# Optimization experiments

Measured on AMD Instinct MI355X. Metric: run time of the kernel, lower is better.

The kernel has to match this reference:

```python
import jax, jax.numpy as jnp
import numpy as np

VOCAB, BLOCK, D, H, L = 50257, 2048, 768, 12, 4
B, T = 1, 2048
DH = D // H


def setup_inputs() -> dict:
    key = jax.random.key(0)
    ks = jax.random.split(key, 16)
    s = 0.02
    return {
        "tokens": jax.random.randint(ks[0], (B, T), 0, VOCAB),
        "wte": jax.random.normal(ks[1], (VOCAB, D), jnp.float32) * s,
        "wpe": jax.random.normal(ks[2], (BLOCK, D), jnp.float32) * s,
        "ln1_w": jnp.ones((L, D), jnp.float32),
        "ln1_b": jnp.zeros((L, D), jnp.float32),
        "qkv_w": jax.random.normal(ks[3], (L, D, 3 * D), jnp.float32) * s,
        "qkv_b": jnp.zeros((L, 3 * D), jnp.float32),
        "proj_w": jax.random.normal(ks[4], (L, D, D), jnp.float32) * s,
        "proj_b": jnp.zeros((L, D), jnp.float32),
        "ln2_w": jnp.ones((L, D), jnp.float32),
        "ln2_b": jnp.zeros((L, D), jnp.float32),
        "fc_w": jax.random.normal(ks[5], (L, D, 4 * D), jnp.float32) * s,
        "fc_b": jnp.zeros((L, 4 * D), jnp.float32),
        "fcp_w": jax.random.normal(ks[6], (L, 4 * D, D), jnp.float32) * s,
        "fcp_b": jnp.zeros((L, D), jnp.float32),
        "lnf_w": jnp.ones((D,), jnp.float32),
        "lnf_b": jnp.zeros((D,), jnp.float32),
    }


def _ln(x, w, b, eps=1e-5):
    m = jnp.mean(x, axis=-1, keepdims=True)
    v = jnp.mean((x - m) ** 2, axis=-1, keepdims=True)
    return (x - m) * jax.lax.rsqrt(v + eps) * w + b


def _attn(x, wq, bq, wp, bp):
    Bq, Tq, _ = x.shape
    qkv = x @ wq + bq  # [B,T,3D]
    q, k, v = jnp.split(qkv, 3, axis=-1)
    q = q.reshape(Bq, Tq, H, DH).transpose(0, 2, 1, 3)  # [B,H,T,dh]
    k = k.reshape(Bq, Tq, H, DH).transpose(0, 2, 1, 3)
    v = v.reshape(Bq, Tq, H, DH).transpose(0, 2, 1, 3)
    w = jnp.einsum("bhqd,bhkd->bhqk", q, k) / np.sqrt(DH).astype(np.float32)
    mask = jnp.tril(jnp.ones((Tq, Tq), bool))
    w = jnp.where(mask, w, -jnp.inf)
    w = jax.nn.softmax(w, axis=-1)
    y = jnp.einsum("bhqk,bhkd->bhqd", w, v)
    y = y.transpose(0, 2, 1, 3).reshape(Bq, Tq, D)
    return y @ wp + bp


def reference(tokens, wte, wpe, ln1_w, ln1_b, qkv_w, qkv_b, proj_w, proj_b,
              ln2_w, ln2_b, fc_w, fc_b, fcp_w, fcp_b, lnf_w, lnf_b):
    x = wte[tokens] + wpe[jnp.arange(tokens.shape[1])]  # [B,T,D]
    for l in range(L):
        x = x + _attn(_ln(x, ln1_w[l], ln1_b[l]), qkv_w[l], qkv_b[l], proj_w[l], proj_b[l])
        h = _ln(x, ln2_w[l], ln2_b[l]) @ fc_w[l] + fc_b[l]
        h = jax.nn.gelu(h, approximate=True)
        x = x + h @ fcp_w[l] + fcp_b[l]
    x = _ln(x, lnf_w, lnf_b)
    logits = x @ wte.T  # tied lm_head, [B,T,V]
    return logits
```

## Files before the change

### kernel.cpp

```cpp
#include <hip/hip_runtime.h>
#include <hip/hip_bf16.h>

#define TSEQ   2048
#define DMODEL 768
#define NHEAD  12
#define DHEAD  64
#define NLAYER 4
#define VOCAB  50257
#define VPAD   50304

typedef __attribute__((ext_vector_type(8))) short short8;
typedef __attribute__((ext_vector_type(4))) float f32x4;
typedef unsigned short ushort_t;

union F8 { short8 v; unsigned long long q[2]; };

__device__ __forceinline__ float b2f(ushort_t u) {
  return __uint_as_float(((unsigned)u) << 16);
}
__device__ __forceinline__ ushort_t f2bu(float f) {
  unsigned u = __float_as_uint(f);
  unsigned r = (u + 0x7fffu + ((u >> 16) & 1u)) >> 16;
  return (ushort_t)r;
}

__device__ __forceinline__ void gload_lds16(const void* g, void* l) {
  __builtin_amdgcn_global_load_lds(
      (const __attribute__((address_space(1))) unsigned int*)g,
      (__attribute__((address_space(3))) unsigned int*)l, 16, 0, 0);
}

__global__ __launch_bounds__(256) void embed_kernel(
    const int* __restrict__ tok, const float* __restrict__ wte,
    const float* __restrict__ wpe, float* __restrict__ x) {
  int i = blockIdx.x * 256 + threadIdx.x;
  int t = i / DMODEL;
  int d = i - t * DMODEL;
  x[i] = wte[tok[t] * DMODEL + d] + wpe[i];
}

__global__ __launch_bounds__(256) void cvt_kernel(
    const float* __restrict__ in, ushort_t* __restrict__ out, int n4) {
  for (int i = blockIdx.x * 256 + threadIdx.x; i < n4; i += gridDim.x * 256) {
    float4 f = reinterpret_cast<const float4*>(in)[i];
    ushort4 o;
    o.x = f2bu(f.x); o.y = f2bu(f.y); o.z = f2bu(f.z); o.w = f2bu(f.w);
    reinterpret_cast<ushort4*>(out)[i] = o;
  }
}

__global__ __launch_bounds__(256) void tcvt_kernel(
    const float* __restrict__ W, ushort_t* __restrict__ Wt, int K, int N,
    long long wstride) {
  W  += (size_t)blockIdx.z * wstride;
  Wt += (size_t)blockIdx.z * wstride;
  __shared__ float Ts[32][33];
  int n0 = blockIdx.x * 32, k0 = blockIdx.y * 32;
  int tx = threadIdx.x & 31, ty = threadIdx.x >> 5;
#pragma unroll
  for (int s = 0; s < 4; ++s)
    Ts[ty + 8 * s][tx] = W[(size_t)(k0 + ty + 8 * s) * N + n0 + tx];
  __syncthreads();
#pragma unroll
  for (int s = 0; s < 4; ++s)
    Wt[(size_t)(n0 + ty + 8 * s) * K + k0 + tx] = f2bu(Ts[tx][ty + 8 * s]);
}

__global__ __launch_bounds__(256) void ln_kernel(
    const float* __restrict__ x, const float* __restrict__ w,
    const float* __restrict__ b, ushort_t* __restrict__ out) {
  int row = blockIdx.x;
  int t = threadIdx.x;
  const float* xr = x + row * DMODEL;
  float v0 = xr[t], v1 = xr[t + 256], v2 = xr[t + 512];
  float s = v0 + v1 + v2;
  float q = v0 * v0 + v1 * v1 + v2 * v2;
#pragma unroll
  for (int off = 32; off >= 1; off >>= 1) {
    s += __shfl_xor(s, off);
    q += __shfl_xor(q, off);
  }
  __shared__ float rs[4], rq[4];
  int wid = t >> 6;
  if ((t & 63) == 0) { rs[wid] = s; rq[wid] = q; }
  __syncthreads();
  s = rs[0] + rs[1] + rs[2] + rs[3];
  q = rq[0] + rq[1] + rq[2] + rq[3];
  float mean = s * (1.f / DMODEL);
  float var  = q * (1.f / DMODEL) - mean * mean;
  float rstd = rsqrtf(var + 1e-5f);
  ushort_t* o = out + row * DMODEL;
  o[t]       = f2bu((v0 - mean) * rstd * w[t]       + b[t]);
  o[t + 256] = f2bu((v1 - mean) * rstd * w[t + 256] + b[t + 256]);
  o[t + 512] = f2bu((v2 - mean) * rstd * w[t + 512] + b[t + 512]);
}

template <int TM, int TN, bool BIAS, bool RES, bool GELU, bool OUTBF16, bool XSWZ>
__global__ __launch_bounds__(256) void mm_kernel(
    const ushort_t* __restrict__ A, const ushort_t* __restrict__ Bt,
    const float* __restrict__ bias, const float* __restrict__ res,
    void* __restrict__ outp, int N, int K, int nrowblk, int nwg) {
  constexpr int HM = TM / 2, HN = TN / 2, FI = TM / 32, FJ = TN / 32;
  constexpr int NCA = TM / 32, NCB = TN / 32;
  __shared__ ushort_t Asm[TM * 64];
  __shared__ ushort_t Bsm[TN * 64];
  const int tid = threadIdx.x;
  const int lane = tid & 63, wid = tid >> 6;
  const int wr = wid >> 1, wc = wid & 1;
  const int l15 = lane & 15, c4 = lane >> 4;
  const int qb0 = (c4 >> 1) << 4;
  const int qb1 = qb0 + 32;
  const int e8 = (c4 & 1) * 8;

  int bid = blockIdx.x;
  if (XSWZ) { int q = nwg >> 3; bid = (bid & 7) * q + (bid >> 3); }
  const int rowb = bid % nrowblk, colb = bid / nrowblk;
  const int rowA0 = rowb * TM, colB0 = colb * TN;

  int ap0[FI], ax[FI], bp0[FJ], bx[FJ];
#pragma unroll
  for (int i = 0; i < FI; ++i) {
    int r = wr * HM + i * 16 + l15;
    ap0[i] = r * 128 + e8; ax[i] = (r & 7) << 4;
  }
#pragma unroll
  for (int j = 0; j < FJ; ++j) {
    int r = wc * HN + j * 16 + l15;
    bp0[j] = r * 128 + e8; bx[j] = (r & 7) << 4;
  }

  const ushort_t* asrc[NCA]; ushort_t* adst[NCA];
  const ushort_t* bsrc[NCB]; ushort_t* bdst[NCB];
#pragma unroll
  for (int s = 0; s < NCA; ++s) {
    int ci = tid + s * 256;
    int row = ci >> 3;
    int logch = (ci & 7) ^ (row & 7);
    asrc[s] = A + (size_t)(rowA0 + row) * K + logch * 8;
    adst[s] = Asm + ci * 8;
  }
#pragma unroll
  for (int s = 0; s < NCB; ++s) {
    int ci = tid + s * 256;
    int row = ci >> 3;
    int logch = (ci & 7) ^ (row & 7);
    bsrc[s] = Bt + (size_t)(colB0 + row) * K + logch * 8;
    bdst[s] = Bsm + ci * 8;
  }

  f32x4 acc[FI][FJ] = {};
  const char* Ab = (const char*)Asm;
  const char* Bb = (const char*)Bsm;

  for (int kt = 0; kt < K; kt += 64) {
    __syncthreads();
#pragma unroll
    for (int s = 0; s < NCA; ++s) gload_lds16(asrc[s] + kt, adst[s]);
#pragma unroll
    for (int s = 0; s < NCB; ++s) gload_lds16(bsrc[s] + kt, bdst[s]);
    __syncthreads();
#pragma unroll
    for (int kk = 0; kk < 2; ++kk) {
      const int k64 = kk * 64;
      short8 a[FI], b[FJ];
#pragma unroll
      for (int i = 0; i < FI; ++i) {
        F8 f;
        f.q[0] = *(const unsigned long long*)(Ab + ap0[i] + ((k64 + qb0) ^ ax[i]));
        f.q[1] = *(const unsigned long long*)(Ab + ap0[i] + ((k64 + qb1) ^ ax[i]));
        a[i] = f.v;
      }
#pragma unroll
      for (int j = 0; j < FJ; ++j) {
        F8 f;
        f.q[0] = *(const unsigned long long*)(Bb + bp0[j] + ((k64 + qb0) ^ bx[j]));
        f.q[1] = *(const unsigned long long*)(Bb + bp0[j] + ((k64 + qb1) ^ bx[j]));
        b[j] = f.v;
      }
#pragma unroll
      for (int i = 0; i < FI; ++i)
#pragma unroll
        for (int j = 0; j < FJ; ++j)
          acc[i][j] = __builtin_amdgcn_mfma_f32_16x16x32_bf16(a[i], b[j], acc[i][j], 0, 0, 0);
    }
  }

#pragma unroll
  for (int i = 0; i < FI; ++i) {
    const int rbase = rowA0 + wr * HM + i * 16 + c4 * 4;
#pragma unroll
    for (int j = 0; j < FJ; ++j) {
      const int col = colB0 + wc * HN + j * 16 + l15;
      if (col < N) {
        float bv = BIAS ? bias[col] : 0.f;
#pragma unroll
        for (int t = 0; t < 4; ++t) {
          float v = acc[i][j][t] + bv;
          if (GELU) {
            float z = 1.5957691216057308f * (v + 0.044715f * v * v * v);
            float th = 1.f - 2.f / (__expf(z) + 1.f);
            v = 0.5f * v * (1.f + th);
          }
          size_t o = (size_t)(rbase + t) * N + col;
          if (RES)          ((float*)outp)[o] = v + res[o];
          else if (OUTBF16) ((ushort_t*)outp)[o] = f2bu(v);
          else              ((float*)outp)[o] = v;
        }
      }
    }
  }
}

__global__ __launch_bounds__(256) void fattn_kernel(
    const ushort_t* __restrict__ qkv, ushort_t* __restrict__ y) {
  const int id = blockIdx.x;
  const int w32 = id / NHEAD;
  const int h = id - w32 * NHEAD;
  const int qb = (w32 & 1) ? (w32 >> 1) : (31 - (w32 >> 1));
  const int q0 = qb * 64;

  __shared__ ushort_t Ksm[64 * 64];
  __shared__ ushort_t Vsm[64 * 64];
  __shared__ ushort_t Psm[4 * 16 * 64];

  const int tid = threadIdx.x;
  const int lane = tid & 63, wv = tid >> 6;
  const int l15 = lane & 15, c4 = lane >> 4;
  const int r7 = l15 & 7;

  const ushort_t* qrow = qkv + (size_t)(q0 + wv * 16 + l15) * (3 * DMODEL) + h * DHEAD;
  const short8 qf0 = *(const short8*)(qrow + c4 * 8);
  const short8 qf1 = *(const short8*)(qrow + 32 + c4 * 8);

  const ushort_t* ksrc[2]; ushort_t* kdst[2];
#pragma unroll
  for (int s = 0; s < 2; ++s) {
    int row = wv * 16 + s * 8 + (lane >> 3);
    int cs = (lane & 7) ^ (row & 7);
    ksrc[s] = qkv + (size_t)row * (3 * DMODEL) + DMODEL + h * DHEAD + cs * 8;
    kdst[s] = Ksm + ((wv * 2 + s) * 64) * 8;
  }
  const int vk = tid & 63, vd0 = (tid >> 6) * 8;
  const ushort_t* vsrc = qkv + (size_t)vk * (3 * DMODEL) + 2 * DMODEL + h * DHEAD;
  const int vkoff = ((vk >> 3) << 3) + (vk & 7);

  float m[4] = {-1e30f, -1e30f, -1e30f, -1e30f};
  float l[4] = {};
  f32x4 acc[4] = {};
  ushort_t* Pw = Psm + wv * 1024;

  for (int k0 = 0; k0 <= q0; k0 += 64) {
    const size_t koff = (size_t)k0 * (3 * DMODEL);
    short8 v0 = *(const short8*)(vsrc + koff + vd0);
    short8 v1 = *(const short8*)(vsrc + koff + vd0 + 32);
    __syncthreads();
#pragma unroll
    for (int s = 0; s < 2; ++s) gload_lds16(ksrc[s] + koff, kdst[s]);
#pragma unroll
    for (int j = 0; j < 8; ++j) {
      int d = vd0 + j;
      Vsm[d * 64 + (vkoff ^ ((d & 7) << 3))] = (ushort_t)v0[j];
      int d2 = d + 32;
      Vsm[d2 * 64 + (vkoff ^ ((d2 & 7) << 3))] = (ushort_t)v1[j];
    }
    __syncthreads();

    f32x4 sv[4];
#pragma unroll
    for (int kt = 0; kt < 4; ++kt) {
      const ushort_t* krow = Ksm + (kt * 16 + l15) * 64;
      short8 kb0 = *(const short8*)(krow + ((c4 ^ r7) << 3));
      short8 kb1 = *(const short8*)(krow + (((4 + c4) ^ r7) << 3));
      f32x4 s = {};
      s = __builtin_amdgcn_mfma_f32_16x16x32_bf16(qf0, kb0, s, 0, 0, 0);
      s = __builtin_amdgcn_mfma_f32_16x16x32_bf16(qf1, kb1, s, 0, 0, 0);
      sv[kt] = s * 0.125f;
    }
    if (k0 == q0) {
#pragma unroll
      for (int kt = 0; kt < 4; ++kt)
#pragma unroll
        for (int r = 0; r < 4; ++r)
          if (kt * 16 + l15 > wv * 16 + c4 * 4 + r) sv[kt][r] = -1e30f;
    }

#pragma unroll
    for (int r = 0; r < 4; ++r) {
      float mv = fmaxf(fmaxf(sv[0][r], sv[1][r]), fmaxf(sv[2][r], sv[3][r]));
      mv = fmaxf(mv, __shfl_xor(mv, 1));
      mv = fmaxf(mv, __shfl_xor(mv, 2));
      mv = fmaxf(mv, __shfl_xor(mv, 4));
      mv = fmaxf(mv, __shfl_xor(mv, 8));
      float nm = fmaxf(m[r], mv);
      float sc = __expf(m[r] - nm);
      m[r] = nm;
      const int row = c4 * 4 + r;
      float sum = 0.f;
#pragma unroll
      for (int kt = 0; kt < 4; ++kt) {
        float p = __expf(sv[kt][r] - nm);
        sum += p;
        Pw[row * 64 + (((kt * 2 + (l15 >> 3)) ^ (row & 7)) << 3) + (l15 & 7)] = f2bu(p);
      }
      sum += __shfl_xor(sum, 1);
      sum += __shfl_xor(sum, 2);
      sum += __shfl_xor(sum, 4);
      sum += __shfl_xor(sum, 8);
      l[r] = l[r] * sc + sum;
#pragma unroll
      for (int j = 0; j < 4; ++j) acc[j][r] *= sc;
    }

    const ushort_t* prow = Pw + l15 * 64;
    short8 pa0 = *(const short8*)(prow + ((c4 ^ r7) << 3));
    short8 pa1 = *(const short8*)(prow + (((4 + c4) ^ r7) << 3));
#pragma unroll
    for (int j = 0; j < 4; ++j) {
      const ushort_t* vrow = Vsm + (j * 16 + l15) * 64;
      short8 vb0 = *(const short8*)(vrow + ((c4 ^ r7) << 3));
      short8 vb1 = *(const short8*)(vrow + (((4 + c4) ^ r7) << 3));
      acc[j] = __builtin_amdgcn_mfma_f32_16x16x32_bf16(pa0, vb0, acc[j], 0, 0, 0);
      acc[j] = __builtin_amdgcn_mfma_f32_16x16x32_bf16(pa1, vb1, acc[j], 0, 0, 0);
    }
  }

  float inv[4];
#pragma unroll
  for (int r = 0; r < 4; ++r) inv[r] = 1.f / l[r];
#pragma unroll
  for (int j = 0; j < 4; ++j)
#pragma unroll
    for (int r = 0; r < 4; ++r)
      y[(size_t)(q0 + wv * 16 + c4 * 4 + r) * DMODEL + h * DHEAD + j * 16 + l15] =
          f2bu(acc[j][r] * inv[r]);
}

extern "C" void kernel_launch(void* const* d_in, const int* in_sizes, int n_in,
                              void* d_out, int out_size, void* d_ws, size_t ws_size,
                              hipStream_t stream) {
  const int*   tokens = (const int*)d_in[0];
  const float* wte    = (const float*)d_in[1];
  const float* wpe    = (const float*)d_in[2];
  const float* ln1_w  = (const float*)d_in[3];
  const float* ln1_b  = (const float*)d_in[4];
  const float* qkv_w  = (const float*)d_in[5];
  const float* qkv_b  = (const float*)d_in[6];
  const float* proj_w = (const float*)d_in[7];
  const float* proj_b = (const float*)d_in[8];
  const float* ln2_w  = (const float*)d_in[9];
  const float* ln2_b  = (const float*)d_in[10];
  const float* fc_w   = (const float*)d_in[11];
  const float* fc_b   = (const float*)d_in[12];
  const float* fcp_w  = (const float*)d_in[13];
  const float* fcp_b  = (const float*)d_in[14];
  const float* lnf_w  = (const float*)d_in[15];
  const float* lnf_b  = (const float*)d_in[16];
  float* out = (float*)d_out;

  char* p = (char*)d_ws;
  auto alloc = [&](size_t bytes) { char* r = p; p += (bytes + 255) & ~(size_t)255; return r; };
  float*    x     = (float*)alloc((size_t)TSEQ * DMODEL * 4);
  ushort_t* lnb   = (ushort_t*)alloc((size_t)TSEQ * DMODEL * 2);
  ushort_t* buf   = (ushort_t*)alloc((size_t)TSEQ * 4 * DMODEL * 2);
  ushort_t* wteb  = (ushort_t*)alloc((size_t)VPAD * DMODEL * 2);
  ushort_t* qkvwt = (ushort_t*)alloc((size_t)NLAYER * 3 * DMODEL * DMODEL * 2);
  ushort_t* projwt= (ushort_t*)alloc((size_t)NLAYER * DMODEL * DMODEL * 2);
  ushort_t* fcwt  = (ushort_t*)alloc((size_t)NLAYER * 4 * DMODEL * DMODEL * 2);
  ushort_t* fcpwt = (ushort_t*)alloc((size_t)NLAYER * 4 * DMODEL * DMODEL * 2);
  ushort_t* qkvb  = buf;
  ushort_t* yb    = buf + (size_t)TSEQ * 3 * DMODEL;
  ushort_t* hfcb  = buf;

  dim3 b256(256);

  cvt_kernel<<<dim3(4096), b256, 0, stream>>>(wte, wteb, VOCAB * DMODEL / 4);
  tcvt_kernel<<<dim3(3 * DMODEL / 32, DMODEL / 32, NLAYER), b256, 0, stream>>>(
      qkv_w, qkvwt, DMODEL, 3 * DMODEL, (long long)3 * DMODEL * DMODEL);
  tcvt_kernel<<<dim3(DMODEL / 32, DMODEL / 32, NLAYER), b256, 0, stream>>>(
      proj_w, projwt, DMODEL, DMODEL, (long long)DMODEL * DMODEL);
  tcvt_kernel<<<dim3(4 * DMODEL / 32, DMODEL / 32, NLAYER), b256, 0, stream>>>(
      fc_w, fcwt, DMODEL, 4 * DMODEL, (long long)4 * DMODEL * DMODEL);
  tcvt_kernel<<<dim3(DMODEL / 32, 4 * DMODEL / 32, NLAYER), b256, 0, stream>>>(
      fcp_w, fcpwt, 4 * DMODEL, DMODEL, (long long)4 * DMODEL * DMODEL);

  embed_kernel<<<dim3(TSEQ * DMODEL / 256), b256, 0, stream>>>(tokens, wte, wpe, x);

  for (int l = 0; l < NLAYER; ++l) {
    ln_kernel<<<dim3(TSEQ), b256, 0, stream>>>(x, ln1_w + l * DMODEL, ln1_b + l * DMODEL, lnb);
    mm_kernel<128, 128, true, false, false, true, false><<<dim3(18 * 16), b256, 0, stream>>>(
        lnb, qkvwt + (size_t)l * 3 * DMODEL * DMODEL, qkv_b + (size_t)l * 3 * DMODEL,
        nullptr, qkvb, 3 * DMODEL, DMODEL, 16, 288);
    fattn_kernel<<<dim3(32 * NHEAD), b256, 0, stream>>>(qkvb, yb);
    mm_kernel<64, 64, true, true, false, false, false><<<dim3(12 * 32), b256, 0, stream>>>(
        yb, projwt + (size_t)l * DMODEL * DMODEL, proj_b + (size_t)l * DMODEL,
        x, x, DMODEL, DMODEL, 32, 384);
    ln_kernel<<<dim3(TSEQ), b256, 0, stream>>>(x, ln2_w + l * DMODEL, ln2_b + l * DMODEL, lnb);
    mm_kernel<128, 128, true, false, true, true, false><<<dim3(24 * 16), b256, 0, stream>>>(
        lnb, fcwt + (size_t)l * 4 * DMODEL * DMODEL, fc_b + (size_t)l * 4 * DMODEL,
        nullptr, hfcb, 4 * DMODEL, DMODEL, 16, 384);
    mm_kernel<64, 64, true, true, false, false, false><<<dim3(12 * 32), b256, 0, stream>>>(
        hfcb, fcpwt + (size_t)l * DMODEL * 4 * DMODEL, fcp_b + (size_t)l * DMODEL,
        x, x, DMODEL, 4 * DMODEL, 32, 384);
  }

  ln_kernel<<<dim3(TSEQ), b256, 0, stream>>>(x, lnf_w, lnf_b, lnb);
  mm_kernel<128, 128, false, false, false, false, true><<<dim3(393 * 16), b256, 0, stream>>>(
      lnb, wteb, nullptr, nullptr, out, VOCAB, DMODEL, 16, 393 * 16);
}
```

Before: 1.085 ms.

## Double-buffer LDS tiles in GEMM kernel with configurable K-tile depth

The GEMM kernel now keeps two LDS buffers for its A and B tiles. It prefetches the next K-tile into the idle buffer while running MFMA on the current one, so each K step needs one barrier instead of two. A BK template parameter is added, with a generalized XOR swizzle for 4 or 8 chunks per row. The 128x128 GEMMs, including the large LM head, use BK=32 so total LDS stays the same, and the 64x64 ones keep BK=64. The cost is twice as many loop iterations and barriers on the 128x128 kernels, and the prefetch depends on the barrier's implicit wait on outstanding loads.

New measurement: 1.106 ms. No clear change (+1.9%).

```diff
diff --git a/kernel.cpp b/kernel.cpp
--- a/kernel.cpp
+++ b/kernel.cpp
@@ -95,21 +95,23 @@
   o[t + 512] = f2bu((v2 - mean) * rstd * w[t + 512] + b[t + 512]);
 }
 
-template <int TM, int TN, bool BIAS, bool RES, bool GELU, bool OUTBF16, bool XSWZ>
+template <int TM, int TN, int BK, bool BIAS, bool RES, bool GELU, bool OUTBF16, bool XSWZ>
 __global__ __launch_bounds__(256) void mm_kernel(
     const ushort_t* __restrict__ A, const ushort_t* __restrict__ Bt,
     const float* __restrict__ bias, const float* __restrict__ res,
     void* __restrict__ outp, int N, int K, int nrowblk, int nwg) {
   constexpr int HM = TM / 2, HN = TN / 2, FI = TM / 32, FJ = TN / 32;
-  constexpr int NCA = TM / 32, NCB = TN / 32;
-  __shared__ ushort_t Asm[TM * 64];
-  __shared__ ushort_t Bsm[TN * 64];
+  constexpr int CH = BK / 8;
+  constexpr int LOGCH = (CH == 4) ? 2 : 3;
+  constexpr int NCA = TM * CH / 256, NCB = TN * CH / 256;
+  constexpr int ABUF = TM * BK, BBUF = TN * BK;
+  __shared__ ushort_t Asm[2][ABUF];
+  __shared__ ushort_t Bsm[2][BBUF];
   const int tid = threadIdx.x;
   const int lane = tid & 63, wid = tid >> 6;
   const int wr = wid >> 1, wc = wid & 1;
   const int l15 = lane & 15, c4 = lane >> 4;
-  const int qb0 = (c4 >> 1) << 4;
-  const int qb1 = qb0 + 32;
+  const int qc = c4 >> 1;
   const int e8 = (c4 & 1) * 8;
 
   int bid = blockIdx.x;
@@ -117,64 +119,74 @@
   const int rowb = bid % nrowblk, colb = bid / nrowblk;
   const int rowA0 = rowb * TM, colB0 = colb * TN;
 
-  int ap0[FI], ax[FI], bp0[FJ], bx[FJ];
+  auto swz = [](int row) { return ((row * CH) >> 3) & (CH - 1); };
+
+  int ap0[FI], axr[FI], bp0[FJ], bxr[FJ];
 #pragma unroll
   for (int i = 0; i < FI; ++i) {
     int r = wr * HM + i * 16 + l15;
-    ap0[i] = r * 128 + e8; ax[i] = (r & 7) << 4;
+    ap0[i] = r * (CH * 16) + e8; axr[i] = swz(r);
   }
 #pragma unroll
   for (int j = 0; j < FJ; ++j) {
     int r = wc * HN + j * 16 + l15;
-    bp0[j] = r * 128 + e8; bx[j] = (r & 7) << 4;
-  }
-
-  const ushort_t* asrc[NCA]; ushort_t* adst[NCA];
-  const ushort_t* bsrc[NCB]; ushort_t* bdst[NCB];
+    bp0[j] = r * (CH * 16) + e8; bxr[j] = swz(r);
+  }
+
+  const ushort_t* asrc[NCA]; int adst[NCA];
+  const ushort_t* bsrc[NCB]; int bdst[NCB];
 #pragma unroll
   for (int s = 0; s < NCA; ++s) {
     int ci = tid + s * 256;
-    int row = ci >> 3;
-    int logch = (ci & 7) ^ (row & 7);
+    int row = ci >> LOGCH;
+    int logch = (ci & (CH - 1)) ^ swz(row);
     asrc[s] = A + (size_t)(rowA0 + row) * K + logch * 8;
-    adst[s] = Asm + ci * 8;
+    adst[s] = ci * 8;
   }
 #pragma unroll
   for (int s = 0; s < NCB; ++s) {
     int ci = tid + s * 256;
-    int row = ci >> 3;
-    int logch = (ci & 7) ^ (row & 7);
+    int row = ci >> LOGCH;
+    int logch = (ci & (CH - 1)) ^ swz(row);
     bsrc[s] = Bt + (size_t)(colB0 + row) * K + logch * 8;
-    bdst[s] = Bsm + ci * 8;
+    bdst[s] = ci * 8;
   }
 
   f32x4 acc[FI][FJ] = {};
-  const char* Ab = (const char*)Asm;
-  const char* Bb = (const char*)Bsm;
-
-  for (int kt = 0; kt < K; kt += 64) {
+  const int nt = K / BK;
+
+#pragma unroll
+  for (int s = 0; s < NCA; ++s) gload_lds16(asrc[s], &Asm[0][adst[s]]);
+#pragma unroll
+  for (int s = 0; s < NCB; ++s) gload_lds16(bsrc[s], &Bsm[0][bdst[s]]);
+
+  for (int t = 0; t < nt; ++t) {
+    const int cur = t & 1;
     __syncthreads();
-#pragma unroll
-    for (int s = 0; s < NCA; ++s) gload_lds16(asrc[s] + kt, adst[s]);
-#pragma unroll
-    for (int s = 0; s < NCB; ++s) gload_lds16(bsrc[s] + kt, bdst[s]);
-    __syncthreads();
-#pragma unroll
-    for (int kk = 0; kk < 2; ++kk) {
-      const int k64 = kk * 64;
+    if (t + 1 < nt) {
+      const int kt = (t + 1) * BK;
+#pragma unroll
+      for (int s = 0; s < NCA; ++s) gload_lds16(asrc[s] + kt, &Asm[cur ^ 1][adst[s]]);
+#pragma unroll
+      for (int s = 0; s < NCB; ++s) gload_lds16(bsrc[s] + kt, &Bsm[cur ^ 1][bdst[s]]);
+    }
+    const char* Ab = (const char*)&Asm[cur][0];
+    const char* Bb = (const char*)&Bsm[cur][0];
+#pragma unroll
+    for (int kk = 0; kk < BK / 32; ++kk) {
       short8 a[FI], b[FJ];
 #pragma unroll
       for (int i = 0; i < FI; ++i) {
         F8 f;
-        f.q[0] = *(const unsigned long long*)(Ab + ap0[i] + ((k64 + qb0) ^ ax[i]));
-        f.q[1] = *(const unsigned long long*)(Ab + ap0[i] + ((k64 + qb1) ^ ax[i]));
+        f.q[0] = *(const unsigned long long*)(Ab + ap0[i] + (((kk * 4 + qc) ^ axr[i]) << 4));
+        f.q[1] = *(const unsigned long long*)(Ab + ap0[i] + (((kk * 4 + qc + 2) ^ axr[i]) << 4));
         a[i] = f.v;
       }
 #pragma unroll
       for (int j = 0; j < FJ; ++j) {
         F8 f;
-        f.q[0] = *(const unsigned long long*)(Bb + bp0[j] + ((k64 + qb0) ^ bx[j]));
-        f.q[1] = *(const unsigned long long*)(Bb + bp0[j] + ((k64 + qb1) ^ bx[j]));
+        f.q[0] = *(const unsigned long long*)(Bb + bp0[j] + (((kk * 4 + qc) ^ bxr[j]) << 4));
+        f.q[1] = *(const unsigned long long*)(Bb + bp0[j] + (((kk * 4 + qc + 2) ^ bxr[j]) << 4));
         b[j] = f.v;
       }
 #pragma unroll
@@ -387,23 +399,23 @@
 
   for (int l = 0; l < NLAYER; ++l) {
     ln_kernel<<<dim3(TSEQ), b256, 0, stream>>>(x, ln1_w + l * DMODEL, ln1_b + l * DMODEL, lnb);
-    mm_kernel<128, 128, true, false, false, true, false><<<dim3(18 * 16), b256, 0, stream>>>(
+    mm_kernel<128, 128, 32, true, false, false, true, false><<<dim3(18 * 16), b256, 0, stream>>>(
         lnb, qkvwt + (size_t)l * 3 * DMODEL * DMODEL, qkv_b + (size_t)l * 3 * DMODEL,
         nullptr, qkvb, 3 * DMODEL, DMODEL, 16, 288);
     fattn_kernel<<<dim3(32 * NHEAD), b256, 0, stream>>>(qkvb, yb);
-    mm_kernel<64, 64, true, true, false, false, false><<<dim3(12 * 32), b256, 0, stream>>>(
+    mm_kernel<64, 64, 64, true, true, false, false, false><<<dim3(12 * 32), b256, 0, stream>>>(
         yb, projwt + (size_t)l * DMODEL * DMODEL, proj_b + (size_t)l * DMODEL,
         x, x, DMODEL, DMODEL, 32, 384);
     ln_kernel<<<dim3(TSEQ), b256, 0, stream>>>(x, ln2_w + l * DMODEL, ln2_b + l * DMODEL, lnb);
-    mm_kernel<128, 128, true, false, true, true, false><<<dim3(24 * 16), b256, 0, stream>>>(
+    mm_kernel<128, 128, 32, true, false, true, true, false><<<dim3(24 * 16), b256, 0, stream>>>(
         lnb, fcwt + (size_t)l * 4 * DMODEL * DMODEL, fc_b + (size_t)l * 4 * DMODEL,
         nullptr, hfcb, 4 * DMODEL, DMODEL, 16, 384);
-    mm_kernel<64, 64, true, true, false, false, false><<<dim3(12 * 32), b256, 0, stream>>>(
+    mm_kernel<64, 64, 64, true, true, false, false, false><<<dim3(12 * 32), b256, 0, stream>>>(
         hfcb, fcpwt + (size_t)l * DMODEL * 4 * DMODEL, fcp_b + (size_t)l * DMODEL,
         x, x, DMODEL, 4 * DMODEL, 32, 384);
   }
 
   ln_kernel<<<dim3(TSEQ), b256, 0, stream>>>(x, lnf_w, lnf_b, lnb);
-  mm_kernel<128, 128, false, false, false, false, true><<<dim3(393 * 16), b256, 0, stream>>>(
+  mm_kernel<128, 128, 32, false, false, false, false, true><<<dim3(393 * 16), b256, 0, stream>>>(
       lnb, wteb, nullptr, nullptr, out, VOCAB, DMODEL, 16, 393 * 16);
 }
```

## Use dedicated 256x256 tiled kernel for LM head logits GEMM

Applied to the files above, without the earlier changes.

Replaces the generic 128x128 GEMM used for the tied LM-head projection with a specialized 512-thread kernel that computes 256x256 output tiles, with 8 waves each owning a 128x64 sub-tile. The larger tile raises arithmetic intensity and reduces redundant reloads of the activation and embedding matrices. The vocab padding is enlarged to a multiple of 256 and the pad rows are zeroed with a memset. A grid remap interleaves workgroups across groups of 8. The kernel is single-buffered with two barriers per K step and carries a large accumulator, so register pressure may limit occupancy.

After: 1.163 ms. 1.07x slower.

```diff
diff --git a/kernel.cpp b/kernel.cpp
--- a/kernel.cpp
+++ b/kernel.cpp
@@ -7,7 +7,7 @@
 #define DHEAD  64
 #define NLAYER 4
 #define VOCAB  50257
-#define VPAD   50304
+#define VPAD   50432
 
 typedef __attribute__((ext_vector_type(8))) short short8;
 typedef __attribute__((ext_vector_type(4))) float f32x4;
@@ -206,6 +206,96 @@
           else if (OUTBF16) ((ushort_t*)outp)[o] = f2bu(v);
           else              ((float*)outp)[o] = v;
         }
+      }
+    }
+  }
+}
+
+__global__ __launch_bounds__(512, 2) void mm256s_kernel(
+    const ushort_t* __restrict__ A, const ushort_t* __restrict__ Bt,
+    float* __restrict__ C, int N, int K, int nrowblk, int nwg) {
+  __shared__ ushort_t Asm[256 * 64];
+  __shared__ ushort_t Bsm[256 * 64];
+  const int tid = threadIdx.x;
+  const int lane = tid & 63, wid = tid >> 6;
+  const int wM = wid >> 2, wN = wid & 3;
+  const int l15 = lane & 15, c4 = lane >> 4;
+  const int qc = c4 >> 1, e8 = (c4 & 1) * 8;
+
+  int bid = blockIdx.x;
+  { int q = nwg >> 3; bid = (bid & 7) * q + (bid >> 3); }
+  const int rowA0 = (bid % nrowblk) * 256;
+  const int colB0 = (bid / nrowblk) * 256;
+
+  const ushort_t* asrc[4]; const ushort_t* bsrc[4]; int dsto[4];
+#pragma unroll
+  for (int s = 0; s < 4; ++s) {
+    int ci = tid + s * 512;
+    int row = ci >> 3;
+    int lg = (ci & 7) ^ (row & 7);
+    asrc[s] = A + (size_t)(rowA0 + row) * K + lg * 8;
+    bsrc[s] = Bt + (size_t)(colB0 + row) * K + lg * 8;
+    dsto[s] = ci * 8;
+  }
+
+  int ap0[8], ax[8], bp0[4], bx[4];
+#pragma unroll
+  for (int i = 0; i < 8; ++i) {
+    int r = wM * 128 + i * 16 + l15;
+    ap0[i] = r * 128 + e8; ax[i] = r & 7;
+  }
+#pragma unroll
+  for (int j = 0; j < 4; ++j) {
+    int r = wN * 64 + j * 16 + l15;
+    bp0[j] = r * 128 + e8; bx[j] = r & 7;
+  }
+
+  f32x4 acc[8][4] = {};
+  const char* Ab = (const char*)Asm;
+  const char* Bb = (const char*)Bsm;
+
+  for (int kt = 0; kt < K; kt += 64) {
+    __syncthreads();
+#pragma unroll
+    for (int s = 0; s < 4; ++s) gload_lds16(asrc[s] + kt, &Asm[dsto[s]]);
+#pragma unroll
+    for (int s = 0; s < 4; ++s) gload_lds16(bsrc[s] + kt, &Bsm[dsto[s]]);
+    __syncthreads();
+#pragma unroll
+    for (int kk = 0; kk < 2; ++kk) {
+      short8 a[8], b[4];
+#pragma unroll
+      for (int i = 0; i < 8; ++i) {
+        F8 f;
+        f.q[0] = *(const unsigned long long*)(Ab + ap0[i] + (((kk * 4 + qc) ^ ax[i]) << 4));
+        f.q[1] = *(const unsigned long long*)(Ab + ap0[i] + (((kk * 4 + qc + 2) ^ ax[i]) << 4));
+        a[i] = f.v;
+      }
+#pragma unroll
+      for (int j = 0; j < 4; ++j) {
+        F8 f;
+        f.q[0] = *(const unsigned long long*)(Bb + bp0[j] + (((kk * 4 + qc) ^ bx[j]) << 4));
+        f.q[1] = *(const unsigned long long*)(Bb + bp0[j] + (((kk * 4 + qc + 2) ^ bx[j]) << 4));
+        b[j] = f.v;
+      }
+#pragma unroll
+      for (int i = 0; i < 8; ++i)
+#pragma unroll
+        for (int j = 0; j < 4; ++j)
+          acc[i][j] = __builtin_amdgcn_mfma_f32_16x16x32_bf16(a[i], b[j], acc[i][j], 0, 0, 0);
+    }
+  }
+
+#pragma unroll
+  for (int i = 0; i < 8; ++i) {
+    const int rbase = rowA0 + wM * 128 + i * 16 + c4 * 4;
+#pragma unroll
+    for (int j = 0; j < 4; ++j) {
+      const int col = colB0 + wN * 64 + j * 16 + l15;
+      if (col < N) {
+#pragma unroll
+        for (int tt = 0; tt < 4; ++tt)
+          C[(size_t)(rbase + tt) * N + col] = acc[i][j][tt];
       }
     }
   }
@@ -373,6 +463,8 @@
 
   dim3 b256(256);
 
+  hipMemsetAsync(wteb + (size_t)VOCAB * DMODEL, 0,
+                 (size_t)(VPAD - VOCAB) * DMODEL * 2, stream);
   cvt_kernel<<<dim3(4096), b256, 0, stream>>>(wte, wteb, VOCAB * DMODEL / 4);
   tcvt_kernel<<<dim3(3 * DMODEL / 32, DMODEL / 32, NLAYER), b256, 0, stream>>>(
       qkv_w, qkvwt, DMODEL, 3 * DMODEL, (long long)3 * DMODEL * DMODEL);
@@ -404,6 +496,6 @@
   }
 
   ln_kernel<<<dim3(TSEQ), b256, 0, stream>>>(x, lnf_w, lnf_b, lnb);
-  mm_kernel<128, 128, false, false, false, false, true><<<dim3(393 * 16), b256, 0, stream>>>(
-      lnb, wteb, nullptr, nullptr, out, VOCAB, DMODEL, 16, 393 * 16);
-}
+  mm256s_kernel<<<dim3(8 * 197), dim3(512), 0, stream>>>(
+      lnb, wteb, out, VOCAB, DMODEL, 8, 8 * 197);
+}
```

## Double-buffer GEMM LDS tiles with async prefetch and vmcnt waits

Applied to the files above, without the earlier changes.

The GEMM kernel now keeps two LDS buffers for the A and B tiles and issues the global-to-LDS loads for the next K tile before computing on the current one. Partial s_waitcnt vmcnt counts plus raw s_barrier calls replace the two __syncthreads per iteration, so load latency can overlap with MFMA work. This doubles LDS use per workgroup, which may lower occupancy, and relies on hand-tuned vmcnt values matching the number of outstanding loads. A memset also zeroes the padded vocab rows of the bf16 embedding copy.

Result: slower. 1.125 ms (+3.7%).

```diff
diff --git a/kernel.cpp b/kernel.cpp
--- a/kernel.cpp
+++ b/kernel.cpp
@@ -102,8 +102,9 @@
     void* __restrict__ outp, int N, int K, int nrowblk, int nwg) {
   constexpr int HM = TM / 2, HN = TN / 2, FI = TM / 32, FJ = TN / 32;
   constexpr int NCA = TM / 32, NCB = TN / 32;
-  __shared__ ushort_t Asm[TM * 64];
-  __shared__ ushort_t Bsm[TN * 64];
+  constexpr int NLD = NCA + NCB;
+  __shared__ ushort_t Asm[2][TM * 64];
+  __shared__ ushort_t Bsm[2][TN * 64];
   const int tid = threadIdx.x;
   const int lane = tid & 63, wid = tid >> 6;
   const int wr = wid >> 1, wc = wid & 1;
@@ -129,15 +130,15 @@
     bp0[j] = r * 128 + e8; bx[j] = (r & 7) << 4;
   }
 
-  const ushort_t* asrc[NCA]; ushort_t* adst[NCA];
-  const ushort_t* bsrc[NCB]; ushort_t* bdst[NCB];
+  const ushort_t* asrc[NCA]; int adst[NCA];
+  const ushort_t* bsrc[NCB]; int bdst[NCB];
 #pragma unroll
   for (int s = 0; s < NCA; ++s) {
     int ci = tid + s * 256;
     int row = ci >> 3;
     int logch = (ci & 7) ^ (row & 7);
     asrc[s] = A + (size_t)(rowA0 + row) * K + logch * 8;
-    adst[s] = Asm + ci * 8;
+    adst[s] = ci * 8;
   }
 #pragma unroll
   for (int s = 0; s < NCB; ++s) {
@@ -145,20 +146,34 @@
     int row = ci >> 3;
     int logch = (ci & 7) ^ (row & 7);
     bsrc[s] = Bt + (size_t)(colB0 + row) * K + logch * 8;
-    bdst[s] = Bsm + ci * 8;
+    bdst[s] = ci * 8;
   }
 
   f32x4 acc[FI][FJ] = {};
-  const char* Ab = (const char*)Asm;
-  const char* Bb = (const char*)Bsm;
-
-  for (int kt = 0; kt < K; kt += 64) {
-    __syncthreads();
-#pragma unroll
-    for (int s = 0; s < NCA; ++s) gload_lds16(asrc[s] + kt, adst[s]);
-#pragma unroll
-    for (int s = 0; s < NCB; ++s) gload_lds16(bsrc[s] + kt, bdst[s]);
-    __syncthreads();
+  const int nt = K / 64;
+
+#pragma unroll
+  for (int s = 0; s < NCA; ++s) gload_lds16(asrc[s], &Asm[0][adst[s]]);
+#pragma unroll
+  for (int s = 0; s < NCB; ++s) gload_lds16(bsrc[s], &Bsm[0][bdst[s]]);
+
+  for (int t = 0; t < nt; ++t) {
+    const int cur = t & 1;
+    if (t + 1 < nt) {
+      const int kt = (t + 1) * 64;
+#pragma unroll
+      for (int s = 0; s < NCA; ++s) gload_lds16(asrc[s] + kt, &Asm[cur ^ 1][adst[s]]);
+#pragma unroll
+      for (int s = 0; s < NCB; ++s) gload_lds16(bsrc[s] + kt, &Bsm[cur ^ 1][bdst[s]]);
+      if constexpr (NLD == 8) asm volatile("s_waitcnt vmcnt(8)" ::: "memory");
+      else                    asm volatile("s_waitcnt vmcnt(4)" ::: "memory");
+    } else {
+      asm volatile("s_waitcnt vmcnt(0)" ::: "memory");
+    }
+    __builtin_amdgcn_s_barrier();
+    asm volatile("" ::: "memory");
+    const char* Ab = (const char*)&Asm[cur][0];
+    const char* Bb = (const char*)&Bsm[cur][0];
 #pragma unroll
     for (int kk = 0; kk < 2; ++kk) {
       const int k64 = kk * 64;
@@ -183,6 +198,8 @@
         for (int j = 0; j < FJ; ++j)
           acc[i][j] = __builtin_amdgcn_mfma_f32_16x16x32_bf16(a[i], b[j], acc[i][j], 0, 0, 0);
     }
+    asm volatile("" ::: "memory");
+    __builtin_amdgcn_s_barrier();
   }
 
 #pragma unroll
@@ -373,6 +390,8 @@
 
   dim3 b256(256);
 
+  hipMemsetAsync(wteb + (size_t)VOCAB * DMODEL, 0,
+                 (size_t)(VPAD - VOCAB) * DMODEL * 2, stream);
   cvt_kernel<<<dim3(4096), b256, 0, stream>>>(wte, wteb, VOCAB * DMODEL / 4);
   tcvt_kernel<<<dim3(3 * DMODEL / 32, DMODEL / 32, NLAYER), b256, 0, stream>>>(
       qkv_w, qkvwt, DMODEL, 3 * DMODEL, (long long)3 * DMODEL * DMODEL);
```
